# Optimization experiments

Hardware: AMD Instinct MI355X
Metric: run time of the kernel (lower is better)

Reference implementation:

```python
import jax, jax.numpy as jnp
import numpy as np

H = 16
D_MODEL = 1024
D_HEAD = D_MODEL // H  # 64


def _xavier(key, shape):
    # xavier_uniform over last two dims (matches torch init on [h, in, out])
    fan_in, fan_out = shape[-2], shape[-1]
    limit = float(np.sqrt(6.0 / (fan_in + fan_out)))
    return jax.random.uniform(key, shape, jnp.float32, -limit, limit)


def setup_inputs() -> dict:
    key = jax.random.key(0)
    ks = jax.random.split(key, 7)
    B, S = 4, 2048
    x_q = jax.random.normal(ks[0], (B, S, D_MODEL), jnp.float32)
    x_k = jax.random.normal(ks[1], (B, S, D_MODEL), jnp.float32)
    x_v = jax.random.normal(ks[2], (B, S, D_MODEL), jnp.float32)
    W_Q = _xavier(ks[3], (H, D_MODEL, D_HEAD))
    W_K = _xavier(ks[4], (H, D_MODEL, D_HEAD))
    W_V = _xavier(ks[5], (H, D_MODEL, D_HEAD))
    # torch Linear weight: [out_features, in_features], y = x @ W^T
    lim = float(np.sqrt(6.0 / (2 * D_MODEL)))  # kaiming-uniform-ish default approximated by xavier for reproducibility
    W_O = jax.random.uniform(ks[6], (D_MODEL, D_MODEL), jnp.float32, -lim, lim)
    return {"x_q": x_q, "x_k": x_k, "x_v": x_v,
            "W_Q": W_Q, "W_K": W_K, "W_V": W_V, "W_O": W_O}


def reference(x_q, x_k, x_v, W_Q, W_K, W_V, W_O):
    d_scale = jnp.asarray(D_HEAD, jnp.float32) ** 0.25  # d_q == d_k == dim_q**(1/4)
    # per-head projections: [b,s,m] x [h,m,d] -> [b,h,s,d]
    Q = jnp.einsum('bsm,hmd->bhsd', x_q, W_Q)
    K = jnp.einsum('bsm,hmd->bhsd', x_k, W_K)
    V = jnp.einsum('bsm,hmd->bhsd', x_v, W_V)
    # column softmax over K^T: shape [b,h,d,s], softmax over dim=-2 (the d axis)
    Kt = jnp.swapaxes(K, -1, -2) / d_scale          # [b,h,d,s]
    Kt = jax.nn.softmax(Kt, axis=-2)
    A = jnp.einsum('bhds,bhse->bhde', Kt, V)        # KV precompute [b,h,d,d]
    Qs = jax.nn.softmax(Q / d_scale, axis=-1)       # row softmax over head dim
    Bt = jnp.einsum('bhsd,bhde->bhse', Qs, A)       # [b,h,s,d]
    b, h, s, d = Bt.shape
    # faithful to torch .view on contiguous [b,h,s,d] -> [b,s,h*d] (pure reshape, no transpose)
    Bt = Bt.reshape(b, s, h * d)
    return jnp.einsum('bsi,oi->bso', Bt, W_O)
```

## Files before the change

### kernel.cpp

```cpp
#include <hip/hip_runtime.h>
#include <cstdint>
#include <cstddef>

#define DMODEL 1024
#define HEADS  16
#define DHEAD  64
#define BATCH  4
#define SEQ    2048
#define ROWS   (BATCH * SEQ)
#define INV_DSCALE 0.3535533905932738f

typedef float  f32x4  __attribute__((ext_vector_type(4)));
typedef __bf16 bf16x8 __attribute__((ext_vector_type(8)));
typedef unsigned short u16x8 __attribute__((ext_vector_type(8)));

__device__ __forceinline__ unsigned short f2bf(float x) {
    union { float f; unsigned u; } c; c.f = x;
    unsigned u = c.u;
    return (unsigned short)((u + 0x7fffu + ((u >> 16) & 1u)) >> 16);
}
__device__ __forceinline__ float bf2f(unsigned short h) {
    union { unsigned u; float f; } c; c.u = ((unsigned)h) << 16;
    return c.f;
}

__device__ __forceinline__ unsigned cvt_pk_bf16(float a, float b) {
#if __has_builtin(__builtin_amdgcn_cvt_pk_bf16_f32)
    typedef __bf16 bf16x2_t __attribute__((ext_vector_type(2)));
    union { bf16x2_t v; unsigned u; } c;
    c.v = __builtin_amdgcn_cvt_pk_bf16_f32(a, b);
    return c.u;
#else
    return (unsigned)f2bf(a) | ((unsigned)f2bf(b) << 16);
#endif
}

__device__ __forceinline__ void load_g2l16(const unsigned short* g, unsigned short* l) {
    __builtin_amdgcn_global_load_lds(
        (const __attribute__((address_space(1))) unsigned int*)g,
        (__attribute__((address_space(3))) unsigned int*)l,
        16 , 0 , 0 );
}

__global__ __launch_bounds__(256) void prep_w(const float* __restrict__ W0,
                                              const float* __restrict__ W1,
                                              const float* __restrict__ W2,
                                              const float* __restrict__ Wo,
                                              unsigned short* __restrict__ T0,
                                              unsigned short* __restrict__ T1,
                                              unsigned short* __restrict__ T2,
                                              unsigned short* __restrict__ To) {
    __shared__ float tile[64][68];
    int blk = blockIdx.x;
    int t = threadIdx.x;
    if (blk < 768) {
        int w = blk >> 8, h = (blk >> 4) & 15, mb = blk & 15;
        const float* W = w == 0 ? W0 : (w == 1 ? W1 : W2);
        unsigned short* T = w == 0 ? T0 : (w == 1 ? T1 : T2);
        #pragma unroll
        for (int i = 0; i < 4; ++i) {
            int f = t + 256 * i;
            int m = f >> 4, dg = (f & 15) * 4;
            *(float4*)&tile[m][dg] = *(const float4*)&W[((size_t)(h * 16 + mb) * 64 + m) * 64 + dg];
        }
        __syncthreads();
        #pragma unroll
        for (int i = 0; i < 2; ++i) {
            int f = t + 256 * i;
            int d = f >> 3, mg = f & 7;
            ushort4 a, b;
            a.x = f2bf(tile[mg * 8 + 0][d]); a.y = f2bf(tile[mg * 8 + 1][d]);
            a.z = f2bf(tile[mg * 8 + 2][d]); a.w = f2bf(tile[mg * 8 + 3][d]);
            b.x = f2bf(tile[mg * 8 + 4][d]); b.y = f2bf(tile[mg * 8 + 5][d]);
            b.z = f2bf(tile[mg * 8 + 6][d]); b.w = f2bf(tile[mg * 8 + 7][d]);
            unsigned short* dst = T + (size_t)(h * 64 + d) * DMODEL + mb * 64 + mg * 8;
            *(ushort4*)dst = a; *(ushort4*)(dst + 4) = b;
        }
    } else {
        int i = (blk - 768) * 256 + t;
        float4 v = ((const float4*)Wo)[i];
        ushort4 o;
        o.x = f2bf(v.x); o.y = f2bf(v.y); o.z = f2bf(v.z); o.w = f2bf(v.w);
        ((ushort4*)To)[i] = o;
    }
}

template <bool OBF16, bool AF32>
__device__ __forceinline__ void gemm_core(const void* __restrict__ Av,
                                          const unsigned short* __restrict__ Bp,
                                          void* __restrict__ Cv,
                                          int K, int N, int bm0, int bn0, bool sm) {
    __shared__ unsigned short ldsA[64 * 64];
    __shared__ unsigned short ldsB[128 * 64];

    const int t    = threadIdx.x;
    const int lane = t & 63;
    const int wave = t >> 6;
    const int wm   = (wave & 1) * 32;
    const int wn   = (wave >> 1) * 64;
    const int fr   = lane & 15;
    const int quad = lane >> 4;

    const float*          A32 = (const float*)Av;
    const unsigned short* A16 = (const unsigned short*)Av;

    f32x4 acc[2][4] = {};

    size_t offA[2];
    #pragma unroll
    for (int i = 0; i < 2; ++i) {
        int f = t + 256 * i, row = f >> 3, kg = (f & 7) ^ (row & 7);
        offA[i] = (size_t)(bm0 + row) * K + kg * 8;
    }
    const unsigned short* gB[4];
    #pragma unroll
    for (int i = 0; i < 4; ++i) {
        int f = t + 256 * i, row = f >> 3, kg = (f & 7) ^ (row & 7);
        gB[i] = Bp + (size_t)(bn0 + row) * K + kg * 8;
    }

    for (int k0 = 0; k0 < K; k0 += 64) {
        if (AF32) {
            #pragma unroll
            for (int i = 0; i < 2; ++i) {
                const float* src = A32 + offA[i] + k0;
                float4 lo = *(const float4*)src;
                float4 hi = *(const float4*)(src + 4);
                uint4 pk;
                pk.x = cvt_pk_bf16(lo.x, lo.y);
                pk.y = cvt_pk_bf16(lo.z, lo.w);
                pk.z = cvt_pk_bf16(hi.x, hi.y);
                pk.w = cvt_pk_bf16(hi.z, hi.w);
                *(uint4*)&ldsA[(t + 256 * i) * 8] = pk;
            }
        } else {
            #pragma unroll
            for (int i = 0; i < 2; ++i)
                load_g2l16(A16 + offA[i] + k0, &ldsA[(t + 256 * i) * 8]);
        }
        #pragma unroll
        for (int i = 0; i < 4; ++i)
            load_g2l16(gB[i] + k0, &ldsB[(t + 256 * i) * 8]);
        asm volatile("s_waitcnt vmcnt(0)" ::: "memory");
        __syncthreads();

        bf16x8 af[2][2], bfr[4][2];
        #pragma unroll
        for (int i = 0; i < 2; ++i) {
            int row = wm + i * 16 + fr;
            #pragma unroll
            for (int kh = 0; kh < 2; ++kh) {
                int s = (kh * 4 + quad) ^ (row & 7);
                af[i][kh] = *reinterpret_cast<const bf16x8*>(&ldsA[row * 64 + s * 8]);
            }
        }
        #pragma unroll
        for (int j = 0; j < 4; ++j) {
            int row = wn + j * 16 + fr;
            #pragma unroll
            for (int kh = 0; kh < 2; ++kh) {
                int s = (kh * 4 + quad) ^ (row & 7);
                bfr[j][kh] = *reinterpret_cast<const bf16x8*>(&ldsB[row * 64 + s * 8]);
            }
        }

        #pragma unroll
        for (int kh = 0; kh < 2; ++kh)
            #pragma unroll
            for (int i = 0; i < 2; ++i)
                #pragma unroll
                for (int j = 0; j < 4; ++j)
                    acc[i][j] = __builtin_amdgcn_mfma_f32_16x16x32_bf16(af[i][kh], bfr[j][kh], acc[i][j], 0, 0, 0);

        __syncthreads();
    }

    #pragma unroll
    for (int i = 0; i < 2; ++i) {
        #pragma unroll
        for (int r = 0; r < 4; ++r) {
            float v[4];
            #pragma unroll
            for (int j = 0; j < 4; ++j) v[j] = acc[i][j][r];
            if (sm) {
                #pragma unroll
                for (int j = 0; j < 4; ++j) v[j] *= INV_DSCALE;
                float m = fmaxf(fmaxf(v[0], v[1]), fmaxf(v[2], v[3]));
                #pragma unroll
                for (int off = 8; off; off >>= 1) m = fmaxf(m, __shfl_xor(m, off, 16));
                float s = 0.f;
                #pragma unroll
                for (int j = 0; j < 4; ++j) { v[j] = __expf(v[j] - m); s += v[j]; }
                #pragma unroll
                for (int off = 8; off; off >>= 1) s += __shfl_xor(s, off, 16);
                float inv = 1.0f / s;
                #pragma unroll
                for (int j = 0; j < 4; ++j) v[j] *= inv;
            }
            int rr = bm0 + wm + i * 16 + quad * 4 + r;
            size_t base = (size_t)rr * N + bn0 + wn + fr;
            if (OBF16) {
                unsigned short* C = (unsigned short*)Cv;
                #pragma unroll
                for (int j = 0; j < 4; ++j) C[base + j * 16] = f2bf(v[j]);
            } else {
                float* C = (float*)Cv;
                #pragma unroll
                for (int j = 0; j < 4; ++j) C[base + j * 16] = v[j];
            }
        }
    }
}

__global__ __launch_bounds__(256, 4) void proj3(const float* __restrict__ xq,
                                                const float* __restrict__ xk,
                                                const float* __restrict__ xv,
                                                const unsigned short* __restrict__ wq,
                                                const unsigned short* __restrict__ wk,
                                                const unsigned short* __restrict__ wv,
                                                unsigned short* __restrict__ Qb,
                                                unsigned short* __restrict__ Kb,
                                                unsigned short* __restrict__ Vb) {
    int z = blockIdx.z;
    const float* A = z == 0 ? xq : (z == 1 ? xk : xv);
    const unsigned short* B = z == 0 ? wq : (z == 1 ? wk : wv);
    unsigned short* C = z == 0 ? Qb : (z == 1 ? Kb : Vb);
    gemm_core<true, true>(A, B, C, DMODEL, DMODEL, blockIdx.x * 64, blockIdx.y * 128, z < 2);
}

__global__ __launch_bounds__(256, 4) void gemm_out(const unsigned short* __restrict__ R,
                                                   const unsigned short* __restrict__ Wo,
                                                   float* __restrict__ out) {
    gemm_core<false, false>(R, Wo, out, DMODEL, DMODEL, blockIdx.x * 64, blockIdx.y * 128, false);
}

__global__ __launch_bounds__(256) void kv_outer(const unsigned short* __restrict__ Ks,
                                                const unsigned short* __restrict__ V,
                                                float* __restrict__ P) {
    __shared__ float sk[64][64];
    __shared__ float sv[64][64];
    int bh = blockIdx.x >> 4, chunk = blockIdx.x & 15;
    int b = bh >> 4, h = bh & 15;
    int t = threadIdx.x;
    int d = t & 63, eg = t >> 6;
    int e0 = eg * 16;
    float acc[16];
    #pragma unroll
    for (int j = 0; j < 16; ++j) acc[j] = 0.f;

    for (int sc = 0; sc < 2; ++sc) {
        int s0 = chunk * 128 + sc * 64;
        #pragma unroll
        for (int i = 0; i < 2; ++i) {
            int f = t + 256 * i;
            int r = f >> 3, c = (f & 7) * 8;
            size_t g = (size_t)(b * SEQ + s0 + r) * DMODEL + h * DHEAD + c;
            u16x8 kk = *(const u16x8*)&Ks[g];
            u16x8 vv = *(const u16x8*)&V[g];
            #pragma unroll
            for (int j = 0; j < 8; ++j) { sk[r][c + j] = bf2f(kk[j]); sv[r][c + j] = bf2f(vv[j]); }
        }
        __syncthreads();
        #pragma unroll 8
        for (int s = 0; s < 64; ++s) {
            float kd = sk[s][d];
            float4 v0 = *(const float4*)&sv[s][e0];
            float4 v1 = *(const float4*)&sv[s][e0 + 4];
            float4 v2 = *(const float4*)&sv[s][e0 + 8];
            float4 v3 = *(const float4*)&sv[s][e0 + 12];
            acc[0]  += kd * v0.x; acc[1]  += kd * v0.y; acc[2]  += kd * v0.z; acc[3]  += kd * v0.w;
            acc[4]  += kd * v1.x; acc[5]  += kd * v1.y; acc[6]  += kd * v1.z; acc[7]  += kd * v1.w;
            acc[8]  += kd * v2.x; acc[9]  += kd * v2.y; acc[10] += kd * v2.z; acc[11] += kd * v2.w;
            acc[12] += kd * v3.x; acc[13] += kd * v3.y; acc[14] += kd * v3.z; acc[15] += kd * v3.w;
        }
        __syncthreads();
    }
    float* Pp = P + ((size_t)chunk * 64 + bh) * 4096 + d * 64 + e0;
    #pragma unroll
    for (int j = 0; j < 16; j += 4)
        *(float4*)&Pp[j] = make_float4(acc[j], acc[j + 1], acc[j + 2], acc[j + 3]);
}

__global__ __launch_bounds__(256) void reduce_A(const float* __restrict__ P,
                                                float* __restrict__ A) {
    int idx = blockIdx.x * 256 + threadIdx.x;
    float s = 0.f;
    #pragma unroll
    for (int c = 0; c < 16; ++c) s += P[(size_t)c * (64 * 4096) + idx];
    A[idx] = s;
}

__global__ __launch_bounds__(256) void qs_a(const unsigned short* __restrict__ Qs,
                                            const float* __restrict__ A,
                                            unsigned short* __restrict__ R) {
    __shared__ float sA[64][64];
    __shared__ float sQ[64][64];
    int bh = blockIdx.x >> 5, sb = blockIdx.x & 31;
    int b = bh >> 4, h = bh & 15;
    int t = threadIdx.x;
    #pragma unroll
    for (int i = 0; i < 4; ++i) {
        int f = t + 256 * i;
        int r = f >> 4, c = (f & 15) * 4;
        *(float4*)&sA[r][c] = *(const float4*)&A[(size_t)bh * 4096 + (size_t)f * 4];
    }
    #pragma unroll
    for (int i = 0; i < 2; ++i) {
        int f = t + 256 * i;
        int r = f >> 3, c = (f & 7) * 8;
        u16x8 q = *(const u16x8*)&Qs[(size_t)(b * SEQ + sb * 64 + r) * DMODEL + h * DHEAD + c];
        #pragma unroll
        for (int j = 0; j < 8; ++j) sQ[r][c + j] = bf2f(q[j]);
    }
    __syncthreads();
    int lane = t & 63, w = t >> 6;
    float acc[16];
    #pragma unroll
    for (int r = 0; r < 16; ++r) acc[r] = 0.f;
    for (int d2 = 0; d2 < 64; d2 += 4) {
        float a0 = sA[d2][lane], a1 = sA[d2 + 1][lane];
        float a2 = sA[d2 + 2][lane], a3 = sA[d2 + 3][lane];
        #pragma unroll
        for (int r = 0; r < 16; ++r) {
            float4 q4 = *(const float4*)&sQ[w * 16 + r][d2];
            acc[r] += q4.x * a0 + q4.y * a1 + q4.z * a2 + q4.w * a3;
        }
    }
    size_t base = (size_t)bh * (SEQ * DHEAD) + (size_t)(sb * 64 + w * 16) * DHEAD + lane;
    #pragma unroll
    for (int r = 0; r < 16; ++r) R[base + (size_t)r * DHEAD] = f2bf(acc[r]);
}

extern "C" void kernel_launch(void* const* d_in, const int* in_sizes, int n_in,
                              void* d_out, int out_size, void* d_ws, size_t ws_size,
                              hipStream_t stream) {
    const float* xq = (const float*)d_in[0];
    const float* xk = (const float*)d_in[1];
    const float* xv = (const float*)d_in[2];
    const float* Wq = (const float*)d_in[3];
    const float* Wk = (const float*)d_in[4];
    const float* Wv = (const float*)d_in[5];
    const float* Wo = (const float*)d_in[6];
    float* out = (float*)d_out;
    char* ws = (char*)d_ws;

    const size_t MB = 1ull << 20;
    unsigned short* wq_t = (unsigned short*)(ws + 0 * MB);
    unsigned short* wk_t = (unsigned short*)(ws + 2 * MB);
    unsigned short* wv_t = (unsigned short*)(ws + 4 * MB);
    unsigned short* wo_b = (unsigned short*)(ws + 6 * MB);
    unsigned short* Qb = (unsigned short*)(ws + 8 * MB);
    unsigned short* Kb = (unsigned short*)(ws + 24 * MB);
    unsigned short* Vb = (unsigned short*)(ws + 40 * MB);
    float* Am = (float*)(ws + 56 * MB);
    unsigned short* R = (unsigned short*)(ws + 57 * MB);
    float* P = (float*)(ws + 73 * MB);

    prep_w<<<1792, 256, 0, stream>>>(Wq, Wk, Wv, Wo, wq_t, wk_t, wv_t, wo_b);

    proj3<<<dim3(ROWS / 64, DMODEL / 128, 3), 256, 0, stream>>>(
        xq, xk, xv, wq_t, wk_t, wv_t, Qb, Kb, Vb);

    kv_outer<<<BATCH * HEADS * 16, 256, 0, stream>>>(Kb, Vb, P);
    reduce_A<<<1024, 256, 0, stream>>>(P, Am);

    qs_a<<<BATCH * HEADS * 32, 256, 0, stream>>>(Qb, Am, R);

    gemm_out<<<dim3(ROWS / 64, DMODEL / 128), 256, 0, stream>>>(R, wo_b, out);
}
```

Measured before the change: 304.4 us.

## Enlarge GEMM tile to 128x128 and remap blocks for XCD-local L2 reuse

Doubles the M tile of the shared GEMM core from 64 to 128 rows, so each wave computes a 64x64 sub-tile with 16 MFMA accumulators and both A and B operands are reused more per LDS load. Block indices are decoded so that consecutive blocks landing on the same XCD share A row-panels, which should improve L2 hit rates. Offsets are narrowed to 32-bit and launch bounds lowered to 3 blocks per SM. The cost is higher register and LDS use per block and half as many blocks, which lowers occupancy.

```diff
diff --git a/kernel.cpp b/kernel.cpp
--- a/kernel.cpp
+++ b/kernel.cpp
@@ -90,13 +90,13 @@
                                           const unsigned short* __restrict__ Bp,
                                           void* __restrict__ Cv,
                                           int K, int N, int bm0, int bn0, bool sm) {
-    __shared__ unsigned short ldsA[64 * 64];
+    __shared__ unsigned short ldsA[128 * 64];
     __shared__ unsigned short ldsB[128 * 64];
 
     const int t    = threadIdx.x;
     const int lane = t & 63;
     const int wave = t >> 6;
-    const int wm   = (wave & 1) * 32;
+    const int wm   = (wave & 1) * 64;
     const int wn   = (wave >> 1) * 64;
     const int fr   = lane & 15;
     const int quad = lane >> 4;
@@ -104,25 +104,20 @@
     const float*          A32 = (const float*)Av;
     const unsigned short* A16 = (const unsigned short*)Av;
 
-    f32x4 acc[2][4] = {};
-
-    size_t offA[2];
-    #pragma unroll
-    for (int i = 0; i < 2; ++i) {
-        int f = t + 256 * i, row = f >> 3, kg = (f & 7) ^ (row & 7);
-        offA[i] = (size_t)(bm0 + row) * K + kg * 8;
-    }
-    const unsigned short* gB[4];
+    f32x4 acc[4][4] = {};
+
+    unsigned offA[4], offB[4];
     #pragma unroll
     for (int i = 0; i < 4; ++i) {
         int f = t + 256 * i, row = f >> 3, kg = (f & 7) ^ (row & 7);
-        gB[i] = Bp + (size_t)(bn0 + row) * K + kg * 8;
+        offA[i] = (unsigned)(bm0 + row) * K + kg * 8;
+        offB[i] = (unsigned)(bn0 + row) * K + kg * 8;
     }
 
     for (int k0 = 0; k0 < K; k0 += 64) {
         if (AF32) {
             #pragma unroll
-            for (int i = 0; i < 2; ++i) {
+            for (int i = 0; i < 4; ++i) {
                 const float* src = A32 + offA[i] + k0;
                 float4 lo = *(const float4*)src;
                 float4 hi = *(const float4*)(src + 4);
@@ -135,48 +130,42 @@
             }
         } else {
             #pragma unroll
-            for (int i = 0; i < 2; ++i)
+            for (int i = 0; i < 4; ++i)
                 load_g2l16(A16 + offA[i] + k0, &ldsA[(t + 256 * i) * 8]);
         }
         #pragma unroll
         for (int i = 0; i < 4; ++i)
-            load_g2l16(gB[i] + k0, &ldsB[(t + 256 * i) * 8]);
+            load_g2l16(Bp + offB[i] + k0, &ldsB[(t + 256 * i) * 8]);
         asm volatile("s_waitcnt vmcnt(0)" ::: "memory");
         __syncthreads();
 
-        bf16x8 af[2][2], bfr[4][2];
-        #pragma unroll
-        for (int i = 0; i < 2; ++i) {
-            int row = wm + i * 16 + fr;
-            #pragma unroll
-            for (int kh = 0; kh < 2; ++kh) {
+        #pragma unroll
+        for (int kh = 0; kh < 2; ++kh) {
+            bf16x8 af[4], bfr[4];
+            #pragma unroll
+            for (int i = 0; i < 4; ++i) {
+                int row = wm + i * 16 + fr;
                 int s = (kh * 4 + quad) ^ (row & 7);
-                af[i][kh] = *reinterpret_cast<const bf16x8*>(&ldsA[row * 64 + s * 8]);
-            }
-        }
-        #pragma unroll
-        for (int j = 0; j < 4; ++j) {
-            int row = wn + j * 16 + fr;
-            #pragma unroll
-            for (int kh = 0; kh < 2; ++kh) {
+                af[i] = *reinterpret_cast<const bf16x8*>(&ldsA[row * 64 + s * 8]);
+            }
+            #pragma unroll
+            for (int j = 0; j < 4; ++j) {
+                int row = wn + j * 16 + fr;
                 int s = (kh * 4 + quad) ^ (row & 7);
-                bfr[j][kh] = *reinterpret_cast<const bf16x8*>(&ldsB[row * 64 + s * 8]);
-            }
-        }
-
-        #pragma unroll
-        for (int kh = 0; kh < 2; ++kh)
-            #pragma unroll
-            for (int i = 0; i < 2; ++i)
+                bfr[j] = *reinterpret_cast<const bf16x8*>(&ldsB[row * 64 + s * 8]);
+            }
+            #pragma unroll
+            for (int i = 0; i < 4; ++i)
                 #pragma unroll
                 for (int j = 0; j < 4; ++j)
-                    acc[i][j] = __builtin_amdgcn_mfma_f32_16x16x32_bf16(af[i][kh], bfr[j][kh], acc[i][j], 0, 0, 0);
-
-        __syncthreads();
-    }
-
-    #pragma unroll
-    for (int i = 0; i < 2; ++i) {
+                    acc[i][j] = __builtin_amdgcn_mfma_f32_16x16x32_bf16(af[i], bfr[j], acc[i][j], 0, 0, 0);
+        }
+
+        __syncthreads();
+    }
+
+    #pragma unroll
+    for (int i = 0; i < 4; ++i) {
         #pragma unroll
         for (int r = 0; r < 4; ++r) {
             float v[4];
@@ -212,7 +201,13 @@
     }
 }
 
-__global__ __launch_bounds__(256, 4) void proj3(const float* __restrict__ xq,
+__device__ __forceinline__ void decode_blk(int flat, int& bm0, int& bn0) {
+    int xcd = flat & 7, idx = flat >> 3;
+    bm0 = (xcd * 8 + (idx >> 3)) * 128;
+    bn0 = (idx & 7) * 128;
+}
+
+__global__ __launch_bounds__(256, 3) void proj3(const float* __restrict__ xq,
                                                 const float* __restrict__ xk,
                                                 const float* __restrict__ xv,
                                                 const unsigned short* __restrict__ wq,
@@ -221,17 +216,21 @@
                                                 unsigned short* __restrict__ Qb,
                                                 unsigned short* __restrict__ Kb,
                                                 unsigned short* __restrict__ Vb) {
-    int z = blockIdx.z;
+    int z = blockIdx.y;
     const float* A = z == 0 ? xq : (z == 1 ? xk : xv);
     const unsigned short* B = z == 0 ? wq : (z == 1 ? wk : wv);
     unsigned short* C = z == 0 ? Qb : (z == 1 ? Kb : Vb);
-    gemm_core<true, true>(A, B, C, DMODEL, DMODEL, blockIdx.x * 64, blockIdx.y * 128, z < 2);
-}
-
-__global__ __launch_bounds__(256, 4) void gemm_out(const unsigned short* __restrict__ R,
+    int bm0, bn0;
+    decode_blk(blockIdx.x, bm0, bn0);
+    gemm_core<true, true>(A, B, C, DMODEL, DMODEL, bm0, bn0, z < 2);
+}
+
+__global__ __launch_bounds__(256, 3) void gemm_out(const unsigned short* __restrict__ R,
                                                    const unsigned short* __restrict__ Wo,
                                                    float* __restrict__ out) {
-    gemm_core<false, false>(R, Wo, out, DMODEL, DMODEL, blockIdx.x * 64, blockIdx.y * 128, false);
+    int bm0, bn0;
+    decode_blk(blockIdx.x, bm0, bn0);
+    gemm_core<false, false>(R, Wo, out, DMODEL, DMODEL, bm0, bn0, false);
 }
 
 __global__ __launch_bounds__(256) void kv_outer(const unsigned short* __restrict__ Ks,
@@ -358,7 +357,7 @@
 
     prep_w<<<1792, 256, 0, stream>>>(Wq, Wk, Wv, Wo, wq_t, wk_t, wv_t, wo_b);
 
-    proj3<<<dim3(ROWS / 64, DMODEL / 128, 3), 256, 0, stream>>>(
+    proj3<<<dim3(512, 3), 256, 0, stream>>>(
         xq, xk, xv, wq_t, wk_t, wv_t, Qb, Kb, Vb);
 
     kv_outer<<<BATCH * HEADS * 16, 256, 0, stream>>>(Kb, Vb, P);
@@ -366,5 +365,5 @@
 
     qs_a<<<BATCH * HEADS * 32, 256, 0, stream>>>(Qb, Am, R);
 
-    gemm_out<<<dim3(ROWS / 64, DMODEL / 128), 256, 0, stream>>>(R, wo_b, out);
-}
+    gemm_out<<<512, 256, 0, stream>>>(R, wo_b, out);
+}
```

Result: slower. 356.4 us (+17.1%).

## Move KV and Qs·A contractions to MFMA with transposed K/V epilogue

Applied to the files above, without the earlier changes.

The projection epilogue now writes K and V transposed per head through LDS, so the KV outer product and the Qs·A product can run as bf16 MFMA tiles instead of scalar FP32 FMA loops. A is stored as bf16 (transposed) and the partial-sum chunk count drops from 16 to 8. Block indices are remapped so that tiles sharing rows land on the same XCD, for L2 locality. This trades extra precision loss in A and a transposing epilogue for far less ALU work in the middle kernels.

```diff
diff --git a/kernel.cpp b/kernel.cpp
--- a/kernel.cpp
+++ b/kernel.cpp
@@ -18,10 +18,6 @@
     union { float f; unsigned u; } c; c.f = x;
     unsigned u = c.u;
     return (unsigned short)((u + 0x7fffu + ((u >> 16) & 1u)) >> 16);
-}
-__device__ __forceinline__ float bf2f(unsigned short h) {
-    union { unsigned u; float f; } c; c.u = ((unsigned)h) << 16;
-    return c.f;
 }
 
 __device__ __forceinline__ unsigned cvt_pk_bf16(float a, float b) {
@@ -85,13 +81,13 @@
     }
 }
 
-template <bool OBF16, bool AF32>
-__device__ __forceinline__ void gemm_core(const void* __restrict__ Av,
+template <bool AF32>
+__device__ __forceinline__ void gemm_tile(const void* __restrict__ Av,
                                           const unsigned short* __restrict__ Bp,
-                                          void* __restrict__ Cv,
-                                          int K, int N, int bm0, int bn0, bool sm) {
-    __shared__ unsigned short ldsA[64 * 64];
-    __shared__ unsigned short ldsB[128 * 64];
+                                          int K, int bm0, int bn0,
+                                          unsigned short* smem, f32x4 acc[2][4]) {
+    unsigned short* ldsA = smem;
+    unsigned short* ldsB = smem + 4096;
 
     const int t    = threadIdx.x;
     const int lane = t & 63;
@@ -104,19 +100,16 @@
     const float*          A32 = (const float*)Av;
     const unsigned short* A16 = (const unsigned short*)Av;
 
-    f32x4 acc[2][4] = {};
-
-    size_t offA[2];
+    unsigned offA[2], offB[4];
     #pragma unroll
     for (int i = 0; i < 2; ++i) {
         int f = t + 256 * i, row = f >> 3, kg = (f & 7) ^ (row & 7);
-        offA[i] = (size_t)(bm0 + row) * K + kg * 8;
-    }
-    const unsigned short* gB[4];
+        offA[i] = (unsigned)(bm0 + row) * K + kg * 8;
+    }
     #pragma unroll
     for (int i = 0; i < 4; ++i) {
         int f = t + 256 * i, row = f >> 3, kg = (f & 7) ^ (row & 7);
-        gB[i] = Bp + (size_t)(bn0 + row) * K + kg * 8;
+        offB[i] = (unsigned)(bn0 + row) * K + kg * 8;
     }
 
     for (int k0 = 0; k0 < K; k0 += 64) {
@@ -140,7 +133,7 @@
         }
         #pragma unroll
         for (int i = 0; i < 4; ++i)
-            load_g2l16(gB[i] + k0, &ldsB[(t + 256 * i) * 8]);
+            load_g2l16(Bp + offB[i] + k0, &ldsB[(t + 256 * i) * 8]);
         asm volatile("s_waitcnt vmcnt(0)" ::: "memory");
         __syncthreads();
 
@@ -163,7 +156,6 @@
                 bfr[j][kh] = *reinterpret_cast<const bf16x8*>(&ldsB[row * 64 + s * 8]);
             }
         }
-
         #pragma unroll
         for (int kh = 0; kh < 2; ++kh)
             #pragma unroll
@@ -174,42 +166,28 @@
 
         __syncthreads();
     }
-
-    #pragma unroll
-    for (int i = 0; i < 2; ++i) {
-        #pragma unroll
-        for (int r = 0; r < 4; ++r) {
-            float v[4];
-            #pragma unroll
-            for (int j = 0; j < 4; ++j) v[j] = acc[i][j][r];
-            if (sm) {
-                #pragma unroll
-                for (int j = 0; j < 4; ++j) v[j] *= INV_DSCALE;
-                float m = fmaxf(fmaxf(v[0], v[1]), fmaxf(v[2], v[3]));
-                #pragma unroll
-                for (int off = 8; off; off >>= 1) m = fmaxf(m, __shfl_xor(m, off, 16));
-                float s = 0.f;
-                #pragma unroll
-                for (int j = 0; j < 4; ++j) { v[j] = __expf(v[j] - m); s += v[j]; }
-                #pragma unroll
-                for (int off = 8; off; off >>= 1) s += __shfl_xor(s, off, 16);
-                float inv = 1.0f / s;
-                #pragma unroll
-                for (int j = 0; j < 4; ++j) v[j] *= inv;
-            }
-            int rr = bm0 + wm + i * 16 + quad * 4 + r;
-            size_t base = (size_t)rr * N + bn0 + wn + fr;
-            if (OBF16) {
-                unsigned short* C = (unsigned short*)Cv;
-                #pragma unroll
-                for (int j = 0; j < 4; ++j) C[base + j * 16] = f2bf(v[j]);
-            } else {
-                float* C = (float*)Cv;
-                #pragma unroll
-                for (int j = 0; j < 4; ++j) C[base + j * 16] = v[j];
-            }
-        }
-    }
+}
+
+__device__ __forceinline__ void softmax4(float v[4]) {
+    #pragma unroll
+    for (int j = 0; j < 4; ++j) v[j] *= INV_DSCALE;
+    float m = fmaxf(fmaxf(v[0], v[1]), fmaxf(v[2], v[3]));
+    #pragma unroll
+    for (int off = 8; off; off >>= 1) m = fmaxf(m, __shfl_xor(m, off, 16));
+    float s = 0.f;
+    #pragma unroll
+    for (int j = 0; j < 4; ++j) { v[j] = __expf(v[j] - m); s += v[j]; }
+    #pragma unroll
+    for (int off = 8; off; off >>= 1) s += __shfl_xor(s, off, 16);
+    float inv = 1.0f / s;
+    #pragma unroll
+    for (int j = 0; j < 4; ++j) v[j] *= inv;
+}
+
+__device__ __forceinline__ void decode_blk(int flat, int& bm0, int& bn0) {
+    int xcd = flat & 7, idx = flat >> 3;
+    bm0 = (xcd * 16 + (idx >> 3)) * 64;
+    bn0 = (idx & 7) * 128;
 }
 
 __global__ __launch_bounds__(256, 4) void proj3(const float* __restrict__ xq,
@@ -219,116 +197,212 @@
                                                 const unsigned short* __restrict__ wk,
                                                 const unsigned short* __restrict__ wv,
                                                 unsigned short* __restrict__ Qb,
-                                                unsigned short* __restrict__ Kb,
-                                                unsigned short* __restrict__ Vb) {
-    int z = blockIdx.z;
+                                                unsigned short* __restrict__ Kt,
+                                                unsigned short* __restrict__ Vt) {
+    __shared__ unsigned short smem[12288];
+    int z = blockIdx.y;
     const float* A = z == 0 ? xq : (z == 1 ? xk : xv);
     const unsigned short* B = z == 0 ? wq : (z == 1 ? wk : wv);
-    unsigned short* C = z == 0 ? Qb : (z == 1 ? Kb : Vb);
-    gemm_core<true, true>(A, B, C, DMODEL, DMODEL, blockIdx.x * 64, blockIdx.y * 128, z < 2);
+    int bm0, bn0;
+    decode_blk(blockIdx.x, bm0, bn0);
+
+    f32x4 acc[2][4] = {};
+    gemm_tile<true>(A, B, DMODEL, bm0, bn0, smem, acc);
+
+    const int t    = threadIdx.x;
+    const int lane = t & 63;
+    const int wave = t >> 6;
+    const int wm   = (wave & 1) * 32;
+    const int wn   = (wave >> 1) * 64;
+    const int fr   = lane & 15;
+    const int quad = lane >> 4;
+    bool do_sm = (z < 2);
+
+    if (z == 0) {
+        #pragma unroll
+        for (int i = 0; i < 2; ++i)
+            #pragma unroll
+            for (int r = 0; r < 4; ++r) {
+                float v[4];
+                #pragma unroll
+                for (int j = 0; j < 4; ++j) v[j] = acc[i][j][r];
+                softmax4(v);
+                int rr = bm0 + wm + i * 16 + quad * 4 + r;
+                size_t base = (size_t)rr * DMODEL + bn0 + wn + fr;
+                #pragma unroll
+                for (int j = 0; j < 4; ++j) Qb[base + j * 16] = f2bf(v[j]);
+            }
+    } else {
+        unsigned short* Ct = smem;
+        #pragma unroll
+        for (int i = 0; i < 2; ++i)
+            #pragma unroll
+            for (int r = 0; r < 4; ++r) {
+                float v[4];
+                #pragma unroll
+                for (int j = 0; j < 4; ++j) v[j] = acc[i][j][r];
+                if (do_sm) softmax4(v);
+                int rr = wm + i * 16 + quad * 4 + r;
+                #pragma unroll
+                for (int j = 0; j < 4; ++j) {
+                    int cc = wn + j * 16 + fr;
+                    Ct[cc * 72 + rr] = f2bf(v[j]);
+                }
+            }
+        __syncthreads();
+        unsigned short* T = (z == 1) ? Kt : Vt;
+        int c = t >> 1, sh = (t & 1) * 32;
+        int col = bn0 + c, h = col >> 6, d = col & 63;
+        int b = bm0 >> 11, s0 = bm0 & 2047;
+        unsigned short* dst = T + (((size_t)(b * 16 + h) * 64 + d) << 11) + s0 + sh;
+        const unsigned short* src = &Ct[c * 72 + sh];
+        #pragma unroll
+        for (int k = 0; k < 4; ++k)
+            *(uint4*)(dst + k * 8) = *(const uint4*)(src + k * 8);
+    }
 }
 
 __global__ __launch_bounds__(256, 4) void gemm_out(const unsigned short* __restrict__ R,
                                                    const unsigned short* __restrict__ Wo,
                                                    float* __restrict__ out) {
-    gemm_core<false, false>(R, Wo, out, DMODEL, DMODEL, blockIdx.x * 64, blockIdx.y * 128, false);
-}
-
-__global__ __launch_bounds__(256) void kv_outer(const unsigned short* __restrict__ Ks,
-                                                const unsigned short* __restrict__ V,
-                                                float* __restrict__ P) {
-    __shared__ float sk[64][64];
-    __shared__ float sv[64][64];
-    int bh = blockIdx.x >> 4, chunk = blockIdx.x & 15;
-    int b = bh >> 4, h = bh & 15;
-    int t = threadIdx.x;
-    int d = t & 63, eg = t >> 6;
-    int e0 = eg * 16;
-    float acc[16];
-    #pragma unroll
-    for (int j = 0; j < 16; ++j) acc[j] = 0.f;
-
-    for (int sc = 0; sc < 2; ++sc) {
-        int s0 = chunk * 128 + sc * 64;
-        #pragma unroll
-        for (int i = 0; i < 2; ++i) {
-            int f = t + 256 * i;
-            int r = f >> 3, c = (f & 7) * 8;
-            size_t g = (size_t)(b * SEQ + s0 + r) * DMODEL + h * DHEAD + c;
-            u16x8 kk = *(const u16x8*)&Ks[g];
-            u16x8 vv = *(const u16x8*)&V[g];
-            #pragma unroll
-            for (int j = 0; j < 8; ++j) { sk[r][c + j] = bf2f(kk[j]); sv[r][c + j] = bf2f(vv[j]); }
-        }
-        __syncthreads();
-        #pragma unroll 8
-        for (int s = 0; s < 64; ++s) {
-            float kd = sk[s][d];
-            float4 v0 = *(const float4*)&sv[s][e0];
-            float4 v1 = *(const float4*)&sv[s][e0 + 4];
-            float4 v2 = *(const float4*)&sv[s][e0 + 8];
-            float4 v3 = *(const float4*)&sv[s][e0 + 12];
-            acc[0]  += kd * v0.x; acc[1]  += kd * v0.y; acc[2]  += kd * v0.z; acc[3]  += kd * v0.w;
-            acc[4]  += kd * v1.x; acc[5]  += kd * v1.y; acc[6]  += kd * v1.z; acc[7]  += kd * v1.w;
-            acc[8]  += kd * v2.x; acc[9]  += kd * v2.y; acc[10] += kd * v2.z; acc[11] += kd * v2.w;
-            acc[12] += kd * v3.x; acc[13] += kd * v3.y; acc[14] += kd * v3.z; acc[15] += kd * v3.w;
-        }
-        __syncthreads();
-    }
-    float* Pp = P + ((size_t)chunk * 64 + bh) * 4096 + d * 64 + e0;
-    #pragma unroll
-    for (int j = 0; j < 16; j += 4)
-        *(float4*)&Pp[j] = make_float4(acc[j], acc[j + 1], acc[j + 2], acc[j + 3]);
+    __shared__ unsigned short smem[12288];
+    int bm0, bn0;
+    decode_blk(blockIdx.x, bm0, bn0);
+    f32x4 acc[2][4] = {};
+    gemm_tile<false>(R, Wo, DMODEL, bm0, bn0, smem, acc);
+
+    const int t = threadIdx.x, lane = t & 63, wave = t >> 6;
+    const int wm = (wave & 1) * 32, wn = (wave >> 1) * 64;
+    const int fr = lane & 15, quad = lane >> 4;
+    #pragma unroll
+    for (int i = 0; i < 2; ++i)
+        #pragma unroll
+        for (int r = 0; r < 4; ++r) {
+            int rr = bm0 + wm + i * 16 + quad * 4 + r;
+            size_t base = (size_t)rr * DMODEL + bn0 + wn + fr;
+            #pragma unroll
+            for (int j = 0; j < 4; ++j) out[base + j * 16] = acc[i][j][r];
+        }
+}
+
+__global__ __launch_bounds__(256) void kv_mfma(const unsigned short* __restrict__ Vt,
+                                               const unsigned short* __restrict__ Kt,
+                                               float* __restrict__ P) {
+    __shared__ unsigned short ldsV[64 * 64];
+    __shared__ unsigned short ldsK[64 * 64];
+    int bh = blockIdx.x >> 3, chunk = blockIdx.x & 7;
+    int t = threadIdx.x, lane = t & 63, wave = t >> 6;
+    int fr = lane & 15, quad = lane >> 4;
+
+    unsigned offV[2], offK[2];
+    #pragma unroll
+    for (int i = 0; i < 2; ++i) {
+        int f = t + 256 * i, row = f >> 3, kg = (f & 7) ^ (row & 7);
+        unsigned o = ((unsigned)(bh * 64 + row) << 11) + chunk * 256 + kg * 8;
+        offV[i] = o; offK[i] = o;
+    }
+
+    f32x4 acc[4] = {};
+    for (int k0 = 0; k0 < 256; k0 += 64) {
+        #pragma unroll
+        for (int i = 0; i < 2; ++i)
+            load_g2l16(Vt + offV[i] + k0, &ldsV[(t + 256 * i) * 8]);
+        #pragma unroll
+        for (int i = 0; i < 2; ++i)
+            load_g2l16(Kt + offK[i] + k0, &ldsK[(t + 256 * i) * 8]);
+        asm volatile("s_waitcnt vmcnt(0)" ::: "memory");
+        __syncthreads();
+
+        #pragma unroll
+        for (int kh = 0; kh < 2; ++kh) {
+            int rowA = wave * 16 + fr;
+            int sA = (kh * 4 + quad) ^ (rowA & 7);
+            bf16x8 av = *reinterpret_cast<const bf16x8*>(&ldsV[rowA * 64 + sA * 8]);
+            #pragma unroll
+            for (int j = 0; j < 4; ++j) {
+                int rowB = j * 16 + fr;
+                int sB = (kh * 4 + quad) ^ (rowB & 7);
+                bf16x8 bv = *reinterpret_cast<const bf16x8*>(&ldsK[rowB * 64 + sB * 8]);
+                acc[j] = __builtin_amdgcn_mfma_f32_16x16x32_bf16(av, bv, acc[j], 0, 0, 0);
+            }
+        }
+        __syncthreads();
+    }
+    float* Pp = P + ((size_t)chunk * 64 + bh) * 4096;
+    #pragma unroll
+    for (int j = 0; j < 4; ++j)
+        #pragma unroll
+        for (int r = 0; r < 4; ++r)
+            Pp[(wave * 16 + quad * 4 + r) * 64 + j * 16 + fr] = acc[j][r];
 }
 
 __global__ __launch_bounds__(256) void reduce_A(const float* __restrict__ P,
-                                                float* __restrict__ A) {
+                                                unsigned short* __restrict__ At) {
     int idx = blockIdx.x * 256 + threadIdx.x;
     float s = 0.f;
     #pragma unroll
-    for (int c = 0; c < 16; ++c) s += P[(size_t)c * (64 * 4096) + idx];
-    A[idx] = s;
-}
-
-__global__ __launch_bounds__(256) void qs_a(const unsigned short* __restrict__ Qs,
-                                            const float* __restrict__ A,
-                                            unsigned short* __restrict__ R) {
-    __shared__ float sA[64][64];
-    __shared__ float sQ[64][64];
-    int bh = blockIdx.x >> 5, sb = blockIdx.x & 31;
+    for (int c = 0; c < 8; ++c) s += P[(size_t)c * (64 * 4096) + idx];
+    At[idx] = f2bf(s);
+}
+
+__global__ __launch_bounds__(256, 4) void qs_mfma(const unsigned short* __restrict__ Qb,
+                                                  const unsigned short* __restrict__ At,
+                                                  unsigned short* __restrict__ R) {
+    __shared__ unsigned short ldsQ[128 * 64];
+    __shared__ unsigned short ldsB[64 * 64];
+    int bh = blockIdx.x >> 4, sb = blockIdx.x & 15;
     int b = bh >> 4, h = bh & 15;
-    int t = threadIdx.x;
+    int t = threadIdx.x, lane = t & 63, wave = t >> 6;
+    int fr = lane & 15, quad = lane >> 4;
+    int wm = wave * 32;
+
     #pragma unroll
     for (int i = 0; i < 4; ++i) {
-        int f = t + 256 * i;
-        int r = f >> 4, c = (f & 15) * 4;
-        *(float4*)&sA[r][c] = *(const float4*)&A[(size_t)bh * 4096 + (size_t)f * 4];
+        int f = t + 256 * i, row = f >> 3, kg = (f & 7) ^ (row & 7);
+        const unsigned short* src = Qb + ((size_t)(b * SEQ + sb * 128 + row) << 10) + h * 64 + kg * 8;
+        load_g2l16(src, &ldsQ[f * 8]);
     }
     #pragma unroll
     for (int i = 0; i < 2; ++i) {
-        int f = t + 256 * i;
-        int r = f >> 3, c = (f & 7) * 8;
-        u16x8 q = *(const u16x8*)&Qs[(size_t)(b * SEQ + sb * 64 + r) * DMODEL + h * DHEAD + c];
-        #pragma unroll
-        for (int j = 0; j < 8; ++j) sQ[r][c + j] = bf2f(q[j]);
-    }
+        int f = t + 256 * i, row = f >> 3, kg = (f & 7) ^ (row & 7);
+        load_g2l16(At + (unsigned)bh * 4096 + row * 64 + kg * 8, &ldsB[f * 8]);
+    }
+    asm volatile("s_waitcnt vmcnt(0)" ::: "memory");
     __syncthreads();
-    int lane = t & 63, w = t >> 6;
-    float acc[16];
-    #pragma unroll
-    for (int r = 0; r < 16; ++r) acc[r] = 0.f;
-    for (int d2 = 0; d2 < 64; d2 += 4) {
-        float a0 = sA[d2][lane], a1 = sA[d2 + 1][lane];
-        float a2 = sA[d2 + 2][lane], a3 = sA[d2 + 3][lane];
-        #pragma unroll
-        for (int r = 0; r < 16; ++r) {
-            float4 q4 = *(const float4*)&sQ[w * 16 + r][d2];
-            acc[r] += q4.x * a0 + q4.y * a1 + q4.z * a2 + q4.w * a3;
-        }
-    }
-    size_t base = (size_t)bh * (SEQ * DHEAD) + (size_t)(sb * 64 + w * 16) * DHEAD + lane;
-    #pragma unroll
-    for (int r = 0; r < 16; ++r) R[base + (size_t)r * DHEAD] = f2bf(acc[r]);
+
+    f32x4 acc[2][4] = {};
+    #pragma unroll
+    for (int kh = 0; kh < 2; ++kh) {
+        bf16x8 af[2], bfr[4];
+        #pragma unroll
+        for (int i = 0; i < 2; ++i) {
+            int row = wm + i * 16 + fr;
+            int s = (kh * 4 + quad) ^ (row & 7);
+            af[i] = *reinterpret_cast<const bf16x8*>(&ldsQ[row * 64 + s * 8]);
+        }
+        #pragma unroll
+        for (int j = 0; j < 4; ++j) {
+            int row = j * 16 + fr;
+            int s = (kh * 4 + quad) ^ (row & 7);
+            bfr[j] = *reinterpret_cast<const bf16x8*>(&ldsB[row * 64 + s * 8]);
+        }
+        #pragma unroll
+        for (int i = 0; i < 2; ++i)
+            #pragma unroll
+            for (int j = 0; j < 4; ++j)
+                acc[i][j] = __builtin_amdgcn_mfma_f32_16x16x32_bf16(af[i], bfr[j], acc[i][j], 0, 0, 0);
+    }
+
+    #pragma unroll
+    for (int i = 0; i < 2; ++i)
+        #pragma unroll
+        for (int r = 0; r < 4; ++r) {
+            int rr = wm + i * 16 + quad * 4 + r;
+            size_t base = ((size_t)bh << 17) + (size_t)(sb * 128 + rr) * 64;
+            #pragma unroll
+            for (int j = 0; j < 4; ++j)
+                R[base + j * 16 + fr] = f2bf(acc[i][j][r]);
+        }
 }
 
 extern "C" void kernel_launch(void* const* d_in, const int* in_sizes, int n_in,
@@ -350,21 +424,20 @@
     unsigned short* wv_t = (unsigned short*)(ws + 4 * MB);
     unsigned short* wo_b = (unsigned short*)(ws + 6 * MB);
     unsigned short* Qb = (unsigned short*)(ws + 8 * MB);
-    unsigned short* Kb = (unsigned short*)(ws + 24 * MB);
-    unsigned short* Vb = (unsigned short*)(ws + 40 * MB);
-    float* Am = (float*)(ws + 56 * MB);
-    unsigned short* R = (unsigned short*)(ws + 57 * MB);
+    unsigned short* Kt = (unsigned short*)(ws + 24 * MB);
+    unsigned short* Vt = (unsigned short*)(ws + 40 * MB);
+    unsigned short* At = (unsigned short*)(ws + 56 * MB);
+    unsigned short* R  = (unsigned short*)(ws + 57 * MB);
     float* P = (float*)(ws + 73 * MB);
 
     prep_w<<<1792, 256, 0, stream>>>(Wq, Wk, Wv, Wo, wq_t, wk_t, wv_t, wo_b);
 
-    proj3<<<dim3(ROWS / 64, DMODEL / 128, 3), 256, 0, stream>>>(
-        xq, xk, xv, wq_t, wk_t, wv_t, Qb, Kb, Vb);
-
-    kv_outer<<<BATCH * HEADS * 16, 256, 0, stream>>>(Kb, Vb, P);
-    reduce_A<<<1024, 256, 0, stream>>>(P, Am);
-
-    qs_a<<<BATCH * HEADS * 32, 256, 0, stream>>>(Qb, Am, R);
-
-    gemm_out<<<dim3(ROWS / 64, DMODEL / 128), 256, 0, stream>>>(R, wo_b, out);
-}
+    proj3<<<dim3(1024, 3), 256, 0, stream>>>(xq, xk, xv, wq_t, wk_t, wv_t, Qb, Kt, Vt);
+
+    kv_mfma<<<BATCH * HEADS * 8, 256, 0, stream>>>(Vt, Kt, P);
+    reduce_A<<<1024, 256, 0, stream>>>(P, At);
+
+    qs_mfma<<<BATCH * HEADS * 16, 256, 0, stream>>>(Qb, At, R);
+
+    gemm_out<<<1024, 256, 0, stream>>>(R, wo_b, out);
+}
```

New measurement: 269.0 us. -11.6%, faster.
